# Performance work log

Hardware: AMD Instinct MI355X
Metric: run time of the kernel (lower is better)

Reference implementation:

```python
import jax, jax.numpy as jnp
import numpy as np

TOP_K = 4  # num_experts_per_tok


def setup_inputs() -> dict:
    key = jax.random.key(0)
    ks = jax.random.split(key, 8)
    B, S, H, E, F = 1, 2048, 2048, 16, 1408
    Fs = 2 * F  # shared expert intermediate = moe_intermediate_size * n_shared_experts
    s = 0.02  # weight init scale for sane numerics
    return {
        "hidden_states": jax.random.normal(ks[0], (B, S, H), jnp.float32),
        "gate_weight": jax.random.normal(ks[1], (E, H), jnp.float32) * s,
        "w_gate": jax.random.normal(ks[2], (E, H, F), jnp.float32) * s,
        "w_up": jax.random.normal(ks[3], (E, H, F), jnp.float32) * s,
        "w_down": jax.random.normal(ks[4], (E, F, H), jnp.float32) * s,
        "ws_gate": jax.random.normal(ks[5], (H, Fs), jnp.float32) * s,
        "ws_up": jax.random.normal(ks[6], (H, Fs), jnp.float32) * s,
        "ws_down": jax.random.normal(ks[7], (Fs, H), jnp.float32) * s,
    }


def reference(hidden_states, gate_weight, w_gate, w_up, w_down, ws_gate, ws_up, ws_down):
    B, S, H = hidden_states.shape
    E = gate_weight.shape[0]
    x = hidden_states.reshape(-1, H)  # [T, H]
    T = x.shape[0]

    # --- gate: fp32 linear, softmax over experts, top-k, scatter to dense mask ---
    logits = jnp.einsum("th,eh->te", x.astype(jnp.float32), gate_weight.astype(jnp.float32))
    probs = jax.nn.softmax(logits, axis=1)
    top_vals, top_idx = jax.lax.top_k(probs, TOP_K)  # [T, K]
    # dense routing weights [T, E]; scatter_add of top-k softmax values (no renorm)
    dense_w = jnp.zeros((T, E), probs.dtype).at[jnp.arange(T)[:, None], top_idx].add(top_vals)

    # --- routed experts: gated SiLU MLP per expert, weighted combine ---
    g = jnp.einsum("th,ehf->tef", x, w_gate)
    u = jnp.einsum("th,ehf->tef", x, w_up)
    a = jax.nn.silu(g) * u  # [T, E, F]
    # fold expert combine into the down projection to avoid a [T, E, H] intermediate
    routed = jnp.einsum("te,tef,efh->th", dense_w.astype(x.dtype), a, w_down)

    # --- shared expert on identity path ---
    shared = jnp.einsum("tf,fh->th", jax.nn.silu(x @ ws_gate) * (x @ ws_up), ws_down)

    out = (routed + shared).reshape(B, S, H)
    return out
```

## Files before the change

kernel.cpp:

```cpp
#include <hip/hip_runtime.h>

#define TT 2048
#define HD 2048
#define FD 1408
#define NE 16
#define NG 18

typedef __attribute__((ext_vector_type(4))) float f32x4;
typedef __attribute__((ext_vector_type(8))) short short8;
typedef __attribute__((ext_vector_type(8))) __bf16 bf16x8;
typedef __attribute__((ext_vector_type(4))) unsigned short u16x4;
typedef __attribute__((ext_vector_type(8))) unsigned short u16x8;

__device__ __forceinline__ unsigned short f2bf(float f) {
  unsigned u = __builtin_bit_cast(unsigned, f);
  u += 0x7fffu + ((u >> 16) & 1u);
  return (unsigned short)(u >> 16);
}

template <typename T>
__device__ __forceinline__ auto mfma_try(T a, T b, f32x4 c, int)
    -> decltype(__builtin_amdgcn_mfma_f32_16x16x32_bf16(a, b, c, 0, 0, 0)) {
  return __builtin_amdgcn_mfma_f32_16x16x32_bf16(a, b, c, 0, 0, 0);
}
template <typename T, typename BV = bf16x8>
__device__ __forceinline__ f32x4 mfma_try(T a, T b, f32x4 c, long) {
  BV aa = __builtin_bit_cast(BV, a);
  BV bb = __builtin_bit_cast(BV, b);
  return __builtin_amdgcn_mfma_f32_16x16x32_bf16(aa, bb, c, 0, 0, 0);
}
__device__ __forceinline__ f32x4 mfma16(short8 a, short8 b, f32x4 c) {
  return mfma_try(a, b, c, 0);
}

__device__ __forceinline__ void gload16(const void* g, void* l) {
  __builtin_amdgcn_global_load_lds(
      (const __attribute__((address_space(1))) void*)g,
      (__attribute__((address_space(3))) void*)l, 16, 0, 0);
}

#define CB1 (FD / 64)
#define CB2 (HD / 128)
#define MAXW1 2464
#define MAXW2 1792

__global__ void gate_kernel(const float* __restrict__ x, const float* __restrict__ gw,
                            float* __restrict__ dense_w) {
  int wid = threadIdx.x >> 6;
  int lane = threadIdx.x & 63;
  int t = blockIdx.x * 4 + wid;
  if (t >= TT) return;
  const float* xr = x + (size_t)t * HD;
  float acc[NE];
#pragma unroll
  for (int e = 0; e < NE; ++e) acc[e] = 0.f;
  for (int h = lane; h < HD; h += 64) {
    float xv = xr[h];
#pragma unroll
    for (int e = 0; e < NE; ++e) acc[e] += xv * gw[e * HD + h];
  }
#pragma unroll
  for (int e = 0; e < NE; ++e) {
    float v = acc[e];
#pragma unroll
    for (int s = 32; s > 0; s >>= 1) v += __shfl_xor(v, s, 64);
    acc[e] = v;
  }
  float mx = acc[0];
#pragma unroll
  for (int e = 1; e < NE; ++e) mx = fmaxf(mx, acc[e]);
  float p[NE]; float sum = 0.f;
#pragma unroll
  for (int e = 0; e < NE; ++e) { p[e] = __expf(acc[e] - mx); sum += p[e]; }
  float inv = 1.f / sum;
#pragma unroll
  for (int e = 0; e < NE; ++e) p[e] *= inv;
  unsigned chosen = 0;
#pragma unroll
  for (int k = 0; k < 4; ++k) {
    int bi = 0; float bv = -1.f;
#pragma unroll
    for (int e = 0; e < NE; ++e) {
      bool ok = !((chosen >> e) & 1) && (p[e] > bv);
      bv = ok ? p[e] : bv;
      bi = ok ? e : bi;
    }
    chosen |= 1u << bi;
  }
  if (lane < NE)
    dense_w[t * NE + lane] = ((chosen >> lane) & 1) ? p[lane] : 0.f;
}

__global__ void build_lists(const float* __restrict__ dense_w, int* __restrict__ tok,
                            float* __restrict__ scale, int* __restrict__ counts) {
  int g = blockIdx.x;
  int lane = threadIdx.x;
  if (g >= NE) {
    for (int i = lane; i < TT; i += 64) { tok[g * TT + i] = i; scale[g * TT + i] = 1.f; }
    if (lane == 0) counts[g] = TT;
    return;
  }
  int base = 0;
  for (int c0 = 0; c0 < TT; c0 += 64) {
    int t = c0 + lane;
    float w = dense_w[t * NE + g];
    bool pred = w > 0.f;
    unsigned long long b = __ballot(pred);
    if (pred) {
      int pos = base + __popcll(b & ((1ull << lane) - 1ull));
      tok[g * TT + pos] = t;
      scale[g * TT + pos] = w;
    }
    base += __popcll(b);
  }
  if (lane == 0) counts[g] = base;
}

__global__ void prefix_kernel(const int* __restrict__ counts, int* __restrict__ rowOff,
                              int* __restrict__ work1, int* __restrict__ work2,
                              int* __restrict__ meta) {
  const int tid = threadIdx.x;
  auto NRB = [&](int g) { return (counts[g] + 127) >> 7; };
  if (tid == 0) {
    int s = 0;
    for (int g = 0; g < NE; ++g) { rowOff[g] = s; s += counts[g]; }
    rowOff[16] = 4 * TT;
    rowOff[17] = 4 * TT + TT;
    int n1 = 0, n2 = 0;
    for (int g = 0; g < NG; ++g) { n1 += NRB(g) * CB1; n2 += NRB(g) * CB2; }
    meta[0] = n1; meta[1] = (n1 + 7) / 8;
    meta[2] = n2; meta[3] = (n2 + 7) / 8;
  }
  if (tid < NG * CB1) {
    int g = tid / CB1, cb = tid % CB1;
    int base = 0;
    for (int gg = 0; gg < g; ++gg) base += NRB(gg) * CB1;
    int n = NRB(g);
    base += cb * n;
    for (int r = 0; r < n; ++r) work1[base + r] = (g << 16) | (cb << 8) | r;
  }
  if (tid < NG * CB2) {
    int g = tid / CB2, cb = tid % CB2;
    int base = 0;
    for (int gg = 0; gg < g; ++gg) base += NRB(gg) * CB2;
    int n = NRB(g);
    base += cb * n;
    for (int r = 0; r < n; ++r) work2[base + r] = (g << 16) | (cb << 8) | r;
  }
}

__global__ void cvt_bf16_kernel(const float* __restrict__ in,
                                unsigned short* __restrict__ out, int n4) {
  int i = blockIdx.x * blockDim.x + threadIdx.x;
  if (i < n4) {
    f32x4 v = ((const f32x4*)in)[i];
    u16x4 h;
    h.x = f2bf(v.x); h.y = f2bf(v.y); h.z = f2bf(v.z); h.w = f2bf(v.w);
    ((u16x4*)out)[i] = h;
  }
}

__global__ __launch_bounds__(256) void transpose_bf16_kernel(
    const float* __restrict__ in, unsigned short* __restrict__ out, int R, int C) {
  __shared__ float tile[64 * 65];
  const size_t base = (size_t)blockIdx.z * R * C;
  const int c0 = blockIdx.x * 64, r0 = blockIdx.y * 64;
  const int tid = threadIdx.x;
  const int rr = tid >> 4;
  const int c4 = (tid & 15) * 4;
#pragma unroll
  for (int it = 0; it < 4; ++it) {
    int r = rr + it * 16;
    f32x4 v = *(const f32x4*)(in + base + (size_t)(r0 + r) * C + c0 + c4);
#pragma unroll
    for (int i = 0; i < 4; ++i) tile[(c4 + i) * 65 + r] = v[i];
  }
  __syncthreads();
  const int cl = tid >> 3;
  const int rc = (tid & 7) * 8;
#pragma unroll
  for (int it = 0; it < 2; ++it) {
    int c = cl + it * 32;
    u16x8 h;
#pragma unroll
    for (int j = 0; j < 8; ++j) h[j] = f2bf(tile[c * 65 + rc + j]);
    *(u16x8*)(out + base + (size_t)(c0 + c) * R + r0 + rc) = h;
  }
}

__global__ __launch_bounds__(256, 4) void gemm1_v7(
    const unsigned short* __restrict__ xb,
    const unsigned short* __restrict__ wgT, const unsigned short* __restrict__ wuT,
    const unsigned short* __restrict__ wsgT, const unsigned short* __restrict__ wsuT,
    const int* __restrict__ tok, const float* __restrict__ scale,
    const int* __restrict__ counts, const int* __restrict__ rowOff,
    const int* __restrict__ work, const int* __restrict__ meta,
    unsigned short* __restrict__ Abuf) {
  const int nw = meta[0], per = meta[1];
  const int xcd = blockIdx.x & 7, slot = blockIdx.x >> 3;
  if (slot >= per) return;
  const int w = xcd * per + slot;
  if (w >= nw) return;
  const int e = work[w];
  const int g = e >> 16, cb = (e >> 8) & 255, rb = e & 255;
  const int count = counts[g];

  __shared__ __align__(16) unsigned short sA[2][128 * 32];
  __shared__ __align__(16) unsigned short sG[2][64 * 32];
  __shared__ __align__(16) unsigned short sU[2][64 * 32];

  const int tid = threadIdx.x, lane = tid & 63, wid = tid >> 6;
  const int wr = (wid >> 1) * 64, wc = (wid & 1) * 32;

  const int lr = lane >> 2, lc = lane & 3;
  const int ra0 = wid * 32 + lr, ra1 = wid * 32 + 16 + lr;
  int gi0 = rb * 128 + ra0, gi1 = rb * 128 + ra1;
  int t0 = (gi0 < count) ? tok[g * TT + gi0] : 0;
  int t1 = (gi1 < count) ? tok[g * TT + gi1] : 0;
  const unsigned short* aG0 = xb + (size_t)t0 * HD + ((lc ^ ((ra0 >> 1) & 3)) * 8);
  const unsigned short* aG1 = xb + (size_t)t1 * HD + ((lc ^ ((ra1 >> 1) & 3)) * 8);
  const int rbb = wid * 16 + lr;
  const unsigned short *bGg, *bGu;
  if (g < NE) {
    size_t o = (size_t)g * FD * HD + (size_t)(cb * 64 + rbb) * HD;
    bGg = wgT + o; bGu = wuT + o;
  } else {
    size_t o = (size_t)((g - NE) * FD + cb * 64 + rbb) * HD;
    bGg = wsgT + o; bGu = wsuT + o;
  }
  const int bco = (lc ^ ((rbb >> 1) & 3)) * 8;
  bGg += bco; bGu += bco;

  const f32x4 fz = {0.f, 0.f, 0.f, 0.f};
  f32x4 accg[4][2], accu[4][2];
#pragma unroll
  for (int m = 0; m < 4; ++m)
#pragma unroll
    for (int n = 0; n < 2; ++n) { accg[m][n] = fz; accu[m][n] = fz; }

  auto STAGEW = [&](int bu, int s) {
    size_t ko = (size_t)s * 32;
    gload16(aG0 + ko, &sA[bu][wid * 1024]);
    gload16(aG1 + ko, &sA[bu][wid * 1024 + 512]);
    gload16(bGg + ko, &sG[bu][wid * 512]);
    gload16(bGu + ko, &sU[bu][wid * 512]);
  };

  auto COMPUTE = [&](int bu) {
    const int ksel = lane >> 4;
    short8 av[4], bg[2], bv[2];
#pragma unroll
    for (int n = 0; n < 2; ++n) {
      int c = wc + n * 16 + (lane & 15);
      int idx = c * 32 + ((ksel ^ ((c >> 1) & 3)) << 3);
      bg[n] = *(const short8*)&sG[bu][idx];
      bv[n] = *(const short8*)&sU[bu][idx];
    }
#pragma unroll
    for (int m = 0; m < 4; ++m) {
      int r = wr + m * 16 + (lane & 15);
      av[m] = *(const short8*)&sA[bu][r * 32 + ((ksel ^ ((r >> 1) & 3)) << 3)];
    }
#pragma unroll
    for (int m = 0; m < 4; ++m)
#pragma unroll
      for (int n = 0; n < 2; ++n) {
        accg[m][n] = mfma16(av[m], bg[n], accg[m][n]);
        accu[m][n] = mfma16(av[m], bv[n], accu[m][n]);
      }
  };

  const int NK = HD / 32;
  STAGEW(0, 0);
  __syncthreads();
  int bu = 0;
#pragma unroll 1
  for (int s = 0; s < NK; ++s) {
    if (s + 1 < NK) STAGEW(bu ^ 1, s + 1);
    COMPUTE(bu);
    __syncthreads();
    bu ^= 1;
  }

  const int rowBase = rowOff[g] + rb * 128;
#pragma unroll
  for (int m = 0; m < 4; ++m)
#pragma unroll
    for (int r = 0; r < 4; ++r) {
      int rl = wr + m * 16 + ((lane >> 4) << 2) + r;
      int gi = rb * 128 + rl;
      if (gi < count) {
        float sc = scale[g * TT + gi];
#pragma unroll
        for (int n = 0; n < 2; ++n) {
          int cl = wc + n * 16 + (lane & 15);
          float gv = accg[m][n][r], uv = accu[m][n][r];
          float a = gv / (1.f + __expf(-gv)) * uv * sc;
          Abuf[(size_t)(rowBase + rl) * FD + cb * 64 + cl] = f2bf(a);
        }
      }
    }
}

__global__ __launch_bounds__(256, 4) void gemm2_v7(
    const unsigned short* __restrict__ Abuf,
    const unsigned short* __restrict__ wdT, const unsigned short* __restrict__ wsdT,
    const int* __restrict__ tok, const int* __restrict__ counts,
    const int* __restrict__ rowOff, const int* __restrict__ work,
    const int* __restrict__ meta, float* __restrict__ out) {
  const int nw = meta[2], per = meta[3];
  const int xcd = blockIdx.x & 7, slot = blockIdx.x >> 3;
  if (slot >= per) return;
  const int w = xcd * per + slot;
  if (w >= nw) return;
  const int e = work[w];
  const int g = e >> 16, cb = (e >> 8) & 255, rb = e & 255;
  const int count = counts[g];

  __shared__ __align__(16) unsigned short sA[2][128 * 32];
  __shared__ __align__(16) unsigned short sB[2][128 * 32];

  const int tid = threadIdx.x, lane = tid & 63, wid = tid >> 6;
  const int wr = (wid >> 1) * 64, wc = (wid & 1) * 64;

  const int rowBase = rowOff[g] + rb * 128;

  const int lr = lane >> 2, lc = lane & 3;
  const int ra0 = wid * 32 + lr, ra1 = wid * 32 + 16 + lr;
  const unsigned short* aG0 =
      Abuf + (size_t)(rowBase + ra0) * FD + ((lc ^ ((ra0 >> 1) & 3)) * 8);
  const unsigned short* aG1 =
      Abuf + (size_t)(rowBase + ra1) * FD + ((lc ^ ((ra1 >> 1) & 3)) * 8);
  const int rb0 = wid * 32 + lr, rb1 = wid * 32 + 16 + lr;
  const unsigned short *bG0, *bG1;
  if (g < NE) {
    bG0 = wdT + (size_t)g * HD * FD + (size_t)(cb * 128 + rb0) * FD;
    bG1 = wdT + (size_t)g * HD * FD + (size_t)(cb * 128 + rb1) * FD;
  } else {
    bG0 = wsdT + (size_t)(cb * 128 + rb0) * (2 * FD) + (size_t)(g - NE) * FD;
    bG1 = wsdT + (size_t)(cb * 128 + rb1) * (2 * FD) + (size_t)(g - NE) * FD;
  }
  bG0 += (lc ^ ((rb0 >> 1) & 3)) * 8;
  bG1 += (lc ^ ((rb1 >> 1) & 3)) * 8;

  const f32x4 fz = {0.f, 0.f, 0.f, 0.f};
  f32x4 acc[4][4];
#pragma unroll
  for (int m = 0; m < 4; ++m)
#pragma unroll
    for (int n = 0; n < 4; ++n) acc[m][n] = fz;

  auto STAGEW = [&](int bu, int s) {
    size_t ko = (size_t)s * 32;
    gload16(aG0 + ko, &sA[bu][wid * 1024]);
    gload16(aG1 + ko, &sA[bu][wid * 1024 + 512]);
    gload16(bG0 + ko, &sB[bu][wid * 1024]);
    gload16(bG1 + ko, &sB[bu][wid * 1024 + 512]);
  };

  auto COMPUTE = [&](int bu) {
    const int ksel = lane >> 4;
    short8 av[4], bv[4];
#pragma unroll
    for (int n = 0; n < 4; ++n) {
      int c = wc + n * 16 + (lane & 15);
      bv[n] = *(const short8*)&sB[bu][c * 32 + ((ksel ^ ((c >> 1) & 3)) << 3)];
    }
#pragma unroll
    for (int m = 0; m < 4; ++m) {
      int r = wr + m * 16 + (lane & 15);
      av[m] = *(const short8*)&sA[bu][r * 32 + ((ksel ^ ((r >> 1) & 3)) << 3)];
    }
#pragma unroll
    for (int m = 0; m < 4; ++m)
#pragma unroll
      for (int n = 0; n < 4; ++n) acc[m][n] = mfma16(av[m], bv[n], acc[m][n]);
  };

  const int NK = FD / 32;
  STAGEW(0, 0);
  __syncthreads();
  int bu = 0;
#pragma unroll 1
  for (int s = 0; s < NK; ++s) {
    if (s + 1 < NK) STAGEW(bu ^ 1, s + 1);
    COMPUTE(bu);
    __syncthreads();
    bu ^= 1;
  }

#pragma unroll
  for (int m = 0; m < 4; ++m)
#pragma unroll
    for (int r = 0; r < 4; ++r) {
      int rl = wr + m * 16 + ((lane >> 4) << 2) + r;
      int gi = rb * 128 + rl;
      if (gi < count) {
        int t = tok[g * TT + gi];
        float* op = out + (size_t)t * HD + cb * 128;
#pragma unroll
        for (int n = 0; n < 4; ++n)
          atomicAdd(op + wc + n * 16 + (lane & 15), acc[m][n][r]);
      }
    }
}

extern "C" void kernel_launch(void* const* d_in, const int* in_sizes, int n_in,
                              void* d_out, int out_size, void* d_ws, size_t ws_size,
                              hipStream_t stream) {
  const float* x      = (const float*)d_in[0];
  const float* gw     = (const float*)d_in[1];
  const float* w_gate = (const float*)d_in[2];
  const float* w_up   = (const float*)d_in[3];
  const float* w_down = (const float*)d_in[4];
  const float* wsg    = (const float*)d_in[5];
  const float* wsu    = (const float*)d_in[6];
  const float* wsd    = (const float*)d_in[7];
  float* out = (float*)d_out;

  char* ws = (char*)d_ws;
  float* dense_w = (float*)(ws);
  int*   tok     = (int*)(ws + (140 << 10));
  float* scale   = (float*)(ws + (290 << 10));
  int*   counts  = (int*)(ws + (440 << 10));
  int*   rowOff  = (int*)(ws + (441 << 10));
  int*   work1   = (int*)(ws + (444 << 10));
  int*   work2   = (int*)(ws + (456 << 10));
  int*   meta    = (int*)(ws + (464 << 10));
  unsigned short* Abuf = (unsigned short*)(ws + (1ull  << 20));
  unsigned short* xb   = (unsigned short*)(ws + (36ull << 20));
  unsigned short* wgT  = (unsigned short*)(ws + (44ull  << 20));
  unsigned short* wuT  = (unsigned short*)(ws + (137ull << 20));
  unsigned short* wdT  = (unsigned short*)(ws + (230ull << 20));
  unsigned short* wsgT = (unsigned short*)(ws + (323ull << 20));
  unsigned short* wsuT = (unsigned short*)(ws + (335ull << 20));
  unsigned short* wsdT = (unsigned short*)(ws + (347ull << 20));

  hipMemsetAsync(d_out, 0, (size_t)out_size * sizeof(float), stream);
  gate_kernel<<<TT / 4, 256, 0, stream>>>(x, gw, dense_w);
  build_lists<<<NG, 64, 0, stream>>>(dense_w, tok, scale, counts);
  prefix_kernel<<<1, 512, 0, stream>>>(counts, rowOff, work1, work2, meta);
  cvt_bf16_kernel<<<(TT * HD / 4 + 255) / 256, 256, 0, stream>>>(x, xb, TT * HD / 4);
  transpose_bf16_kernel<<<dim3(FD / 64, HD / 64, NE), 256, 0, stream>>>(w_gate, wgT, HD, FD);
  transpose_bf16_kernel<<<dim3(FD / 64, HD / 64, NE), 256, 0, stream>>>(w_up,   wuT, HD, FD);
  transpose_bf16_kernel<<<dim3(HD / 64, FD / 64, NE), 256, 0, stream>>>(w_down, wdT, FD, HD);
  transpose_bf16_kernel<<<dim3(2 * FD / 64, HD / 64, 1), 256, 0, stream>>>(wsg, wsgT, HD, 2 * FD);
  transpose_bf16_kernel<<<dim3(2 * FD / 64, HD / 64, 1), 256, 0, stream>>>(wsu, wsuT, HD, 2 * FD);
  transpose_bf16_kernel<<<dim3(HD / 64, 2 * FD / 64, 1), 256, 0, stream>>>(wsd, wsdT, 2 * FD, HD);

  gemm1_v7<<<MAXW1, 256, 0, stream>>>(
      xb, wgT, wuT, wsgT, wsuT, tok, scale, counts, rowOff, work1, meta, Abuf);
  gemm2_v7<<<MAXW2, 256, 0, stream>>>(
      Abuf, wdT, wsdT, tok, counts, rowOff, work2, meta, out);
}
```

Before: 582.0 us.

## Fuse fp32 weight transpose and bf16 conversion into GEMM B-tile staging

Removes the six separate transpose_bf16 kernels and has both grouped GEMMs read the fp32 weights directly. Each thread loads them into registers, packs pairs along K into bf16, and writes them into swizzled LDS tiles, with the register prefetch running two stages ahead. This avoids writing and re-reading a full bf16 copy of every weight matrix. The cost is that weights are now read as fp32 (twice the bytes) and repeatedly by several row blocks, and the kernels spend more VGPRs and ALU work on conversion inside the main loop.

```diff
diff --git a/kernel.cpp b/kernel.cpp
--- a/kernel.cpp
+++ b/kernel.cpp
@@ -11,11 +11,15 @@
 typedef __attribute__((ext_vector_type(8))) __bf16 bf16x8;
 typedef __attribute__((ext_vector_type(4))) unsigned short u16x4;
 typedef __attribute__((ext_vector_type(8))) unsigned short u16x8;
+typedef __attribute__((ext_vector_type(2))) unsigned int u32x2;
 
 __device__ __forceinline__ unsigned short f2bf(float f) {
   unsigned u = __builtin_bit_cast(unsigned, f);
   u += 0x7fffu + ((u >> 16) & 1u);
   return (unsigned short)(u >> 16);
+}
+__device__ __forceinline__ unsigned pack2(float lo, float hi) {
+  return (unsigned)f2bf(lo) | ((unsigned)f2bf(hi) << 16);
 }
 
 template <typename T>
@@ -160,38 +164,10 @@
   }
 }
 
-__global__ __launch_bounds__(256) void transpose_bf16_kernel(
-    const float* __restrict__ in, unsigned short* __restrict__ out, int R, int C) {
-  __shared__ float tile[64 * 65];
-  const size_t base = (size_t)blockIdx.z * R * C;
-  const int c0 = blockIdx.x * 64, r0 = blockIdx.y * 64;
-  const int tid = threadIdx.x;
-  const int rr = tid >> 4;
-  const int c4 = (tid & 15) * 4;
-#pragma unroll
-  for (int it = 0; it < 4; ++it) {
-    int r = rr + it * 16;
-    f32x4 v = *(const f32x4*)(in + base + (size_t)(r0 + r) * C + c0 + c4);
-#pragma unroll
-    for (int i = 0; i < 4; ++i) tile[(c4 + i) * 65 + r] = v[i];
-  }
-  __syncthreads();
-  const int cl = tid >> 3;
-  const int rc = (tid & 7) * 8;
-#pragma unroll
-  for (int it = 0; it < 2; ++it) {
-    int c = cl + it * 32;
-    u16x8 h;
-#pragma unroll
-    for (int j = 0; j < 8; ++j) h[j] = f2bf(tile[c * 65 + rc + j]);
-    *(u16x8*)(out + base + (size_t)(c0 + c) * R + r0 + rc) = h;
-  }
-}
-
-__global__ __launch_bounds__(256, 4) void gemm1_v7(
+__global__ __launch_bounds__(256, 4) void gemm1_v8(
     const unsigned short* __restrict__ xb,
-    const unsigned short* __restrict__ wgT, const unsigned short* __restrict__ wuT,
-    const unsigned short* __restrict__ wsgT, const unsigned short* __restrict__ wsuT,
+    const float* __restrict__ w_gate, const float* __restrict__ w_up,
+    const float* __restrict__ ws_gate, const float* __restrict__ ws_up,
     const int* __restrict__ tok, const float* __restrict__ scale,
     const int* __restrict__ counts, const int* __restrict__ rowOff,
     const int* __restrict__ work, const int* __restrict__ meta,
@@ -219,17 +195,23 @@
   int t1 = (gi1 < count) ? tok[g * TT + gi1] : 0;
   const unsigned short* aG0 = xb + (size_t)t0 * HD + ((lc ^ ((ra0 >> 1) & 3)) * 8);
   const unsigned short* aG1 = xb + (size_t)t1 * HD + ((lc ^ ((ra1 >> 1) & 3)) * 8);
-  const int rbb = wid * 16 + lr;
-  const unsigned short *bGg, *bGu;
+
+  const int kp = tid >> 4, n0 = (tid & 15) * 4;
+  const float *Bg, *Bu; size_t ldb; int bcol0;
   if (g < NE) {
-    size_t o = (size_t)g * FD * HD + (size_t)(cb * 64 + rbb) * HD;
-    bGg = wgT + o; bGu = wuT + o;
+    size_t o = (size_t)g * HD * FD;
+    Bg = w_gate + o; Bu = w_up + o; ldb = FD; bcol0 = cb * 64;
   } else {
-    size_t o = (size_t)((g - NE) * FD + cb * 64 + rbb) * HD;
-    bGg = wsgT + o; bGu = wsuT + o;
-  }
-  const int bco = (lc ^ ((rbb >> 1) & 3)) * 8;
-  bGg += bco; bGu += bco;
+    Bg = ws_gate; Bu = ws_up; ldb = 2 * FD; bcol0 = (g - NE) * FD + cb * 64;
+  }
+  const float* gp = Bg + (size_t)(2 * kp) * ldb + bcol0 + n0;
+  const float* up = Bu + (size_t)(2 * kp) * ldb + bcol0 + n0;
+  int bwi[4];
+#pragma unroll
+  for (int j = 0; j < 4; ++j) {
+    int n = n0 + j;
+    bwi[j] = n * 16 + (((kp >> 2) ^ ((n >> 2) & 3)) << 2) + (kp & 3);
+  }
 
   const f32x4 fz = {0.f, 0.f, 0.f, 0.f};
   f32x4 accg[4][2], accu[4][2];
@@ -238,12 +220,27 @@
 #pragma unroll
     for (int n = 0; n < 2; ++n) { accg[m][n] = fz; accu[m][n] = fz; }
 
-  auto STAGEW = [&](int bu, int s) {
+  f32x4 g0, g1, u0, u1;
+
+  auto STAGEA = [&](int bu, int s) {
     size_t ko = (size_t)s * 32;
     gload16(aG0 + ko, &sA[bu][wid * 1024]);
     gload16(aG1 + ko, &sA[bu][wid * 1024 + 512]);
-    gload16(bGg + ko, &sG[bu][wid * 512]);
-    gload16(bGu + ko, &sU[bu][wid * 512]);
+  };
+  auto LOADB = [&](int s) {
+    const float* _g = gp + (size_t)s * 32 * ldb;
+    const float* _u = up + (size_t)s * 32 * ldb;
+    g0 = *(const f32x4*)_g; g1 = *(const f32x4*)(_g + ldb);
+    u0 = *(const f32x4*)_u; u1 = *(const f32x4*)(_u + ldb);
+  };
+  auto STOREB = [&](int bu) {
+    unsigned* gw_ = (unsigned*)sG[bu];
+    unsigned* uw_ = (unsigned*)sU[bu];
+#pragma unroll
+    for (int j = 0; j < 4; ++j) {
+      gw_[bwi[j]] = pack2(g0[j], g1[j]);
+      uw_[bwi[j]] = pack2(u0[j], u1[j]);
+    }
   };
 
   auto COMPUTE = [&](int bu) {
@@ -252,7 +249,7 @@
 #pragma unroll
     for (int n = 0; n < 2; ++n) {
       int c = wc + n * 16 + (lane & 15);
-      int idx = c * 32 + ((ksel ^ ((c >> 1) & 3)) << 3);
+      int idx = c * 32 + ((ksel ^ ((c >> 2) & 3)) << 3);
       bg[n] = *(const short8*)&sG[bu][idx];
       bv[n] = *(const short8*)&sU[bu][idx];
     }
@@ -271,15 +268,19 @@
   };
 
   const int NK = HD / 32;
-  STAGEW(0, 0);
+  LOADB(0);
+  STAGEA(0, 0);
+  STOREB(0);
+  LOADB(1);
   __syncthreads();
-  int bu = 0;
 #pragma unroll 1
   for (int s = 0; s < NK; ++s) {
-    if (s + 1 < NK) STAGEW(bu ^ 1, s + 1);
+    int bu = s & 1;
+    if (s + 1 < NK) STAGEA(bu ^ 1, s + 1);
     COMPUTE(bu);
+    if (s + 1 < NK) STOREB(bu ^ 1);
+    if (s + 2 < NK) LOADB(s + 2);
     __syncthreads();
-    bu ^= 1;
   }
 
   const int rowBase = rowOff[g] + rb * 128;
@@ -302,9 +303,9 @@
     }
 }
 
-__global__ __launch_bounds__(256, 4) void gemm2_v7(
+__global__ __launch_bounds__(256, 4) void gemm2_v8(
     const unsigned short* __restrict__ Abuf,
-    const unsigned short* __restrict__ wdT, const unsigned short* __restrict__ wsdT,
+    const float* __restrict__ w_down, const float* __restrict__ ws_down,
     const int* __restrict__ tok, const int* __restrict__ counts,
     const int* __restrict__ rowOff, const int* __restrict__ work,
     const int* __restrict__ meta, float* __restrict__ out) {
@@ -331,17 +332,19 @@
       Abuf + (size_t)(rowBase + ra0) * FD + ((lc ^ ((ra0 >> 1) & 3)) * 8);
   const unsigned short* aG1 =
       Abuf + (size_t)(rowBase + ra1) * FD + ((lc ^ ((ra1 >> 1) & 3)) * 8);
-  const int rb0 = wid * 32 + lr, rb1 = wid * 32 + 16 + lr;
-  const unsigned short *bG0, *bG1;
-  if (g < NE) {
-    bG0 = wdT + (size_t)g * HD * FD + (size_t)(cb * 128 + rb0) * FD;
-    bG1 = wdT + (size_t)g * HD * FD + (size_t)(cb * 128 + rb1) * FD;
-  } else {
-    bG0 = wsdT + (size_t)(cb * 128 + rb0) * (2 * FD) + (size_t)(g - NE) * FD;
-    bG1 = wsdT + (size_t)(cb * 128 + rb1) * (2 * FD) + (size_t)(g - NE) * FD;
-  }
-  bG0 += (lc ^ ((rb0 >> 1) & 3)) * 8;
-  bG1 += (lc ^ ((rb1 >> 1) & 3)) * 8;
+
+  const int kg = tid >> 5, n0 = (tid & 31) * 4;
+  const float* bp;
+  if (g < NE)
+    bp = w_down + (size_t)g * FD * HD + (size_t)(4 * kg) * HD + cb * 128 + n0;
+  else
+    bp = ws_down + (size_t)((g - NE) * FD + 4 * kg) * HD + cb * 128 + n0;
+  int bwi[4];
+#pragma unroll
+  for (int j = 0; j < 4; ++j) {
+    int n = n0 + j;
+    bwi[j] = n * 16 + (((kg >> 1) ^ ((n >> 2) & 3)) << 2) + ((2 * kg) & 3);
+  }
 
   const f32x4 fz = {0.f, 0.f, 0.f, 0.f};
   f32x4 acc[4][4];
@@ -350,12 +353,29 @@
 #pragma unroll
     for (int n = 0; n < 4; ++n) acc[m][n] = fz;
 
-  auto STAGEW = [&](int bu, int s) {
+  f32x4 b0, b1, b2, b3;
+
+  auto STAGEA = [&](int bu, int s) {
     size_t ko = (size_t)s * 32;
     gload16(aG0 + ko, &sA[bu][wid * 1024]);
     gload16(aG1 + ko, &sA[bu][wid * 1024 + 512]);
-    gload16(bG0 + ko, &sB[bu][wid * 1024]);
-    gload16(bG1 + ko, &sB[bu][wid * 1024 + 512]);
+  };
+  auto LOADB = [&](int s) {
+    const float* _b = bp + (size_t)s * 32 * HD;
+    b0 = *(const f32x4*)_b;
+    b1 = *(const f32x4*)(_b + HD);
+    b2 = *(const f32x4*)(_b + 2 * HD);
+    b3 = *(const f32x4*)(_b + 3 * HD);
+  };
+  auto STOREB = [&](int bu) {
+    unsigned* bw_ = (unsigned*)sB[bu];
+#pragma unroll
+    for (int j = 0; j < 4; ++j) {
+      u32x2 v;
+      v.x = pack2(b0[j], b1[j]);
+      v.y = pack2(b2[j], b3[j]);
+      *(u32x2*)&bw_[bwi[j]] = v;
+    }
   };
 
   auto COMPUTE = [&](int bu) {
@@ -364,7 +384,7 @@
 #pragma unroll
     for (int n = 0; n < 4; ++n) {
       int c = wc + n * 16 + (lane & 15);
-      bv[n] = *(const short8*)&sB[bu][c * 32 + ((ksel ^ ((c >> 1) & 3)) << 3)];
+      bv[n] = *(const short8*)&sB[bu][c * 32 + ((ksel ^ ((c >> 2) & 3)) << 3)];
     }
 #pragma unroll
     for (int m = 0; m < 4; ++m) {
@@ -378,15 +398,19 @@
   };
 
   const int NK = FD / 32;
-  STAGEW(0, 0);
+  LOADB(0);
+  STAGEA(0, 0);
+  STOREB(0);
+  LOADB(1);
   __syncthreads();
-  int bu = 0;
 #pragma unroll 1
   for (int s = 0; s < NK; ++s) {
-    if (s + 1 < NK) STAGEW(bu ^ 1, s + 1);
+    int bu = s & 1;
+    if (s + 1 < NK) STAGEA(bu ^ 1, s + 1);
     COMPUTE(bu);
+    if (s + 1 < NK) STOREB(bu ^ 1);
+    if (s + 2 < NK) LOADB(s + 2);
     __syncthreads();
-    bu ^= 1;
   }
 
 #pragma unroll
@@ -429,27 +453,15 @@
   int*   meta    = (int*)(ws + (464 << 10));
   unsigned short* Abuf = (unsigned short*)(ws + (1ull  << 20));
   unsigned short* xb   = (unsigned short*)(ws + (36ull << 20));
-  unsigned short* wgT  = (unsigned short*)(ws + (44ull  << 20));
-  unsigned short* wuT  = (unsigned short*)(ws + (137ull << 20));
-  unsigned short* wdT  = (unsigned short*)(ws + (230ull << 20));
-  unsigned short* wsgT = (unsigned short*)(ws + (323ull << 20));
-  unsigned short* wsuT = (unsigned short*)(ws + (335ull << 20));
-  unsigned short* wsdT = (unsigned short*)(ws + (347ull << 20));
 
   hipMemsetAsync(d_out, 0, (size_t)out_size * sizeof(float), stream);
   gate_kernel<<<TT / 4, 256, 0, stream>>>(x, gw, dense_w);
   build_lists<<<NG, 64, 0, stream>>>(dense_w, tok, scale, counts);
   prefix_kernel<<<1, 512, 0, stream>>>(counts, rowOff, work1, work2, meta);
   cvt_bf16_kernel<<<(TT * HD / 4 + 255) / 256, 256, 0, stream>>>(x, xb, TT * HD / 4);
-  transpose_bf16_kernel<<<dim3(FD / 64, HD / 64, NE), 256, 0, stream>>>(w_gate, wgT, HD, FD);
-  transpose_bf16_kernel<<<dim3(FD / 64, HD / 64, NE), 256, 0, stream>>>(w_up,   wuT, HD, FD);
-  transpose_bf16_kernel<<<dim3(HD / 64, FD / 64, NE), 256, 0, stream>>>(w_down, wdT, FD, HD);
-  transpose_bf16_kernel<<<dim3(2 * FD / 64, HD / 64, 1), 256, 0, stream>>>(wsg, wsgT, HD, 2 * FD);
-  transpose_bf16_kernel<<<dim3(2 * FD / 64, HD / 64, 1), 256, 0, stream>>>(wsu, wsuT, HD, 2 * FD);
-  transpose_bf16_kernel<<<dim3(HD / 64, 2 * FD / 64, 1), 256, 0, stream>>>(wsd, wsdT, 2 * FD, HD);
-
-  gemm1_v7<<<MAXW1, 256, 0, stream>>>(
-      xb, wgT, wuT, wsgT, wsuT, tok, scale, counts, rowOff, work1, meta, Abuf);
-  gemm2_v7<<<MAXW2, 256, 0, stream>>>(
-      Abuf, wdT, wsdT, tok, counts, rowOff, work2, meta, out);
-}
+
+  gemm1_v8<<<MAXW1, 256, 0, stream>>>(
+      xb, w_gate, w_up, wsg, wsu, tok, scale, counts, rowOff, work1, meta, Abuf);
+  gemm2_v8<<<MAXW2, 256, 0, stream>>>(
+      Abuf, w_down, wsd, tok, counts, rowOff, work2, meta, out);
+}
```

Measured after the change: 510.4 us. 1.14x faster.
